# Optimization experiments

Measured on AMD Instinct MI355X. Metric: run time of the kernel, lower is better.

## Reference

```python
import jax, jax.numpy as jnp
import numpy as np

DROP_P = 0.1  # module default dropout


def setup_inputs() -> dict:
    key = jax.random.key(0)
    kq, kk, kv = jax.random.split(key, 3)
    B, L, H = 4, 4096, 64
    return {
        "q": jax.random.normal(kq, (B, L, H), dtype=jnp.float32),
        "k": jax.random.normal(kk, (B, L, H), dtype=jnp.float32),
        "v": jax.random.normal(kv, (B, L, H), dtype=jnp.float32),
    }


def reference(q, k, v):
    # q: [B, ql, H], k: [B, kl, H], v: [B, kl, H]
    H = q.shape[-1]
    scale = 1.0 / jnp.sqrt(jnp.asarray(H, dtype=q.dtype))
    # [B, ql, kl] score matrix (materialized, as in the original module)
    scores = jnp.einsum('bqh,bkh->bqk', q, k) * scale
    ql, kl = scores.shape[1], scores.shape[2]
    causal = jnp.tril(jnp.ones((ql, kl), dtype=bool))  # self.tril[:ql, :kl]
    scores = jnp.where(causal[None, :, :], scores, -jnp.inf)
    wei = jax.nn.softmax(scores, axis=-1)
    # deterministic dropout (train-mode path in the torch module)
    keep_p = 1.0 - DROP_P
    keep = jax.random.bernoulli(jax.random.key(42), keep_p, wei.shape)
    wei = jnp.where(keep, wei / keep_p, jnp.zeros((), dtype=wei.dtype))
    return jnp.einsum('bqk,bkh->bqh', wei, v)
```

## Files before the change

kernel.cpp:

```cpp
#include <hip/hip_runtime.h>

#define LQ   4096
#define HDIM 64
#define KEEP_LIMIT (7549747u << 9)
#define SCALE_LOG2E 0.18033688011112042f

typedef __attribute__((ext_vector_type(8))) short short8v;
typedef __attribute__((ext_vector_type(4))) short short4v;
typedef __attribute__((ext_vector_type(4))) float f32x4;

__device__ __forceinline__ unsigned rotl32(unsigned x, int r) {
  return (x << r) | (x >> (32 - r));
}

__device__ __forceinline__ float keep_sel(unsigned j, float e) {
  const unsigned ks1 = 42u;
  const unsigned ks2 = 0x1BD11BDAu ^ 42u;
  unsigned x0 = 0u, x1 = j + ks1;
#define TFR(r) { x0 += x1; x1 = rotl32(x1, r); x1 ^= x0; }
  TFR(13) TFR(15) TFR(26) TFR(6)   x0 += ks1; x1 += ks2 + 1u;
  TFR(17) TFR(29) TFR(16) TFR(24)  x0 += ks2; x1 += 0u  + 2u;
  TFR(13) TFR(15) TFR(26) TFR(6)   x0 += 0u;  x1 += ks1 + 3u;
  TFR(17) TFR(29) TFR(16) TFR(24)  x0 += ks1; x1 += ks2 + 4u;
  TFR(13) TFR(15) TFR(26) TFR(6)   x0 += ks2; x1 += 0u  + 5u;
#undef TFR
  return ((x0 ^ x1) < KEEP_LIMIT) ? e : 0.f;
}

__device__ __forceinline__ unsigned short f2bf(float x) {
  unsigned u = __float_as_uint(x);
  u += 0x7fffu + ((u >> 16) & 1u);
  return (unsigned short)(u >> 16);
}

__device__ __forceinline__ void gload16(const void* g, void* l) {
  __builtin_amdgcn_global_load_lds(
      (const __attribute__((address_space(1))) unsigned int*)g,
      (__attribute__((address_space(3))) unsigned int*)l, 16, 0, 0);
}

#if __has_builtin(__builtin_amdgcn_mfma_f32_16x16x16bf16_1k)
#define MFMA16(a, b, c) __builtin_amdgcn_mfma_f32_16x16x16bf16_1k(a, b, c, 0, 0, 0)
#else
__device__ __forceinline__ f32x4 mfma16_asm(short4v a, short4v b, f32x4 c) {
  f32x4 d;
  asm volatile("v_mfma_f32_16x16x16_bf16 %0, %1, %2, %3"
               : "=v"(d) : "v"(a), "v"(b), "v"(c));
  return d;
}
#define MFMA16(a, b, c) mfma16_asm(a, b, c)
#endif

__global__ __launch_bounds__(256) void prep(const float* __restrict__ k,
                                            const float* __restrict__ v,
                                            unsigned short* __restrict__ kb,
                                            unsigned short* __restrict__ vtb) {
  __shared__ float t[64][65];
  const int b = blockIdx.y, tl = blockIdx.x;
  const int tid = threadIdx.x, lane = tid & 63, grp = tid >> 6;
  {
    const float* kp = k + ((size_t)b * LQ + tl * 64) * HDIM;
    unsigned short* kbp = kb + ((size_t)b * LQ + tl * 64) * HDIM;
#pragma unroll
    for (int i = 0; i < 4; i++) {
      int e = (i * 256 + tid) * 4;
      float4 x = *(const float4*)(kp + e);
      ushort4 y;
      y.x = f2bf(x.x); y.y = f2bf(x.y); y.z = f2bf(x.z); y.w = f2bf(x.w);
      *(ushort4*)(kbp + e) = y;
    }
  }
#pragma unroll
  for (int c = 0; c < 16; c++) {
    int r = c * 4 + grp;
    t[r][lane] = v[((size_t)b * LQ + tl * 64 + r) * HDIM + lane];
  }
  __syncthreads();
#pragma unroll
  for (int c = 0; c < 16; c++) {
    int h = c * 4 + grp;
    vtb[((size_t)b * HDIM + h) * LQ + tl * 64 + lane] = f2bf(t[lane][h]);
  }
}

__global__ __launch_bounds__(256, 4) void attn(
    const float* __restrict__ q, const unsigned short* __restrict__ kb,
    const unsigned short* __restrict__ vtb, float* __restrict__ o,
    float* __restrict__ plsum) {
  __shared__ __align__(16) unsigned short vl[4][64 * 64];

  const int bx = blockIdx.x;
  const int tile16 = 255 - (bx >> 3);
  const int b = (bx >> 1) & 3;
  const int s = bx & 1;
  const int tid = threadIdx.x, lane = tid & 63, wq = tid >> 6;
  const int g = lane >> 4, r = lane & 15;
  const int qrow = tile16 * 16 + r;
  const int nt = (tile16 >> 2) + 1;
  const int half = (nt + 1) >> 1;
  const int ts = s ? half : 0, te = s ? nt : half;
  const int ntm1 = nt - 1;
  const unsigned sw = (unsigned)((r & 7) << 4);
  const unsigned jq = ((unsigned)b << 24) | ((unsigned)qrow << 12);
  const f32x4 zero4 = (f32x4){0.f, 0.f, 0.f, 0.f};

  short8v qf0, qf1;
  {
    const float* qp = q + ((size_t)b * LQ + qrow) * HDIM + g * 8;
    float4 a0 = *(const float4*)qp;
    float4 a1 = *(const float4*)(qp + 4);
    float4 b0 = *(const float4*)(qp + 32);
    float4 b1 = *(const float4*)(qp + 36);
    qf0[0] = (short)f2bf(a0.x); qf0[1] = (short)f2bf(a0.y);
    qf0[2] = (short)f2bf(a0.z); qf0[3] = (short)f2bf(a0.w);
    qf0[4] = (short)f2bf(a1.x); qf0[5] = (short)f2bf(a1.y);
    qf0[6] = (short)f2bf(a1.z); qf0[7] = (short)f2bf(a1.w);
    qf1[0] = (short)f2bf(b0.x); qf1[1] = (short)f2bf(b0.y);
    qf1[2] = (short)f2bf(b0.z); qf1[3] = (short)f2bf(b0.w);
    qf1[4] = (short)f2bf(b1.x); qf1[5] = (short)f2bf(b1.y);
    qf1[6] = (short)f2bf(b1.z); qf1[7] = (short)f2bf(b1.w);
  }

  const char* vt_b = (const char*)vtb + (size_t)b * HDIM * LQ * 2;
  const char* vpA;
  const char* vpB;
  {
    unsigned d0 = (unsigned)(tid * 16);
    unsigned d1 = d0 + 4096u;
    unsigned vsrc0 = (d0 >> 7) * (LQ * 2) + ((d0 & 127u) ^ (((d0 >> 7) & 7u) << 4));
    unsigned vsrc1 = (d1 >> 7) * (LQ * 2) + ((d1 & 127u) ^ (((d1 >> 7) & 7u) << 4));
    vpA = vt_b + vsrc0 + (size_t)ts * 128;
    vpB = vt_b + vsrc1 + (size_t)ts * 128;
  }
  const char* kp =
      (const char*)kb + ((size_t)b * LQ + wq * 16 + r) * 128 + g * 16 +
      (size_t)ts * 8192;

  char* const lw = (char*)&vl[0][0] + wq * 1024;

  f32x4 acc[4];
  acc[0] = zero4; acc[1] = zero4; acc[2] = zero4; acc[3] = zero4;
  float lsum = 0.f;

  const int n = te - ts;
  short8v kA0 = {}, kA1 = {}, kB0 = {}, kB1 = {};
  if (n > 0) {
    gload16(vpA, lw);
    gload16(vpB, lw + 4096);
    kA0 = *(const short8v*)(kp);
    kA1 = *(const short8v*)(kp + 64);
  }
  if (n > 1) {
    gload16(vpA + 128, lw + 8192);
    gload16(vpB + 128, lw + 8192 + 4096);
    kB0 = *(const short8v*)(kp + 8192);
    kB1 = *(const short8v*)(kp + 8192 + 64);
  }
  kp += 16384;
  __syncthreads();

#define COMPUTE_TILE(K0, K1, BUFI, T, DIAG)                                    \
  {                                                                            \
    const char* vlp = (const char*)&vl[BUFI][0] + r * 128 +                    \
                      (((unsigned)(wq * 32 + g * 8)) ^ sw);                    \
    short4v vf[4];                                                             \
    _Pragma("unroll") for (int hg = 0; hg < 4; ++hg)                           \
        vf[hg] = *(const short4v*)(vlp + hg * 2048);                           \
    f32x4 S = __builtin_amdgcn_mfma_f32_16x16x32_bf16(K0, qf0, zero4, 0, 0, 0);\
    S = __builtin_amdgcn_mfma_f32_16x16x32_bf16(K1, qf1, S, 0, 0, 0);          \
    const int kvb = (T) * 64 + wq * 16 + g * 4;                                \
    float w[4];                                                                \
    if (DIAG) {                                                                \
      _Pragma("unroll") for (int reg = 0; reg < 4; ++reg) {                    \
        float e = (kvb + reg <= qrow) ? exp2f(S[reg] * SCALE_LOG2E) : 0.f;     \
        lsum += e;                                                             \
        w[reg] = keep_sel(jq | (unsigned)(kvb + reg), e);                      \
      }                                                                        \
    } else {                                                                   \
      _Pragma("unroll") for (int reg = 0; reg < 4; ++reg) {                    \
        float e = exp2f(S[reg] * SCALE_LOG2E);                                 \
        lsum += e;                                                             \
        w[reg] = keep_sel(jq | (unsigned)(kvb + reg), e);                      \
      }                                                                        \
    }                                                                          \
    union { unsigned u[2]; short4v s4; } pu;                                   \
    asm("v_cvt_pk_bf16_f32 %0, %1, %2" : "=v"(pu.u[0]) : "v"(w[0]), "v"(w[1]));\
    asm("v_cvt_pk_bf16_f32 %0, %1, %2" : "=v"(pu.u[1]) : "v"(w[2]), "v"(w[3]));\
    const short4v pa = pu.s4;                                                  \
    _Pragma("unroll") for (int hg = 0; hg < 4; ++hg)                           \
        acc[hg] = MFMA16(pa, vf[hg], acc[hg]);                                 \
  }

  int t = ts;
  int base = 0;
  for (; t + 2 <= te; t += 2) {
    short8v nA0 = kA0, nA1 = kA1, nB0 = kB0, nB1 = kB1;
    char* const lwn = lw + (base ^ 2) * 8192;
    if (t + 2 < te) {
      gload16(vpA + 256, lwn);
      gload16(vpB + 256, lwn + 4096);
      nA0 = *(const short8v*)(kp);
      nA1 = *(const short8v*)(kp + 64);
    }
    if (t + 3 < te) {
      gload16(vpA + 384, lwn + 8192);
      gload16(vpB + 384, lwn + 8192 + 4096);
      nB0 = *(const short8v*)(kp + 8192);
      nB1 = *(const short8v*)(kp + 8192 + 64);
    }

    COMPUTE_TILE(kA0, kA1, base, t, false)
    COMPUTE_TILE(kB0, kB1, base + 1, t + 1, (t + 1) == ntm1)

    __syncthreads();
    kA0 = nA0; kA1 = nA1; kB0 = nB0; kB1 = nB1;
    vpA += 256; vpB += 256; kp += 16384;
    base ^= 2;
  }
  if (t < te) {
    COMPUTE_TILE(kA0, kA1, base, t, t == ntm1)
  }
#undef COMPUTE_TILE

  lsum += __shfl_xor(lsum, 16);
  lsum += __shfl_xor(lsum, 32);
  if (lane < 16)
    atomicAdd(&plsum[b * LQ + tile16 * 16 + lane], lsum);

  float* ob = o + ((size_t)b * LQ + tile16 * 16) * HDIM;
#pragma unroll
  for (int hg = 0; hg < 4; ++hg)
#pragma unroll
    for (int reg = 0; reg < 4; ++reg)
      atomicAdd(&ob[(g * 4 + reg) * HDIM + hg * 16 + r], acc[hg][reg]);
}

__global__ __launch_bounds__(256) void norm(float* __restrict__ o,
                                            const float* __restrict__ plsum) {
  const int idx = blockIdx.x * 256 + threadIdx.x;
  f32x4 x = ((const f32x4*)o)[idx];
  const float inv = 1.0f / (plsum[idx >> 4] * 0.9f);
  ((f32x4*)o)[idx] = x * inv;
}

extern "C" void kernel_launch(void* const* d_in, const int* in_sizes, int n_in,
                              void* d_out, int out_size, void* d_ws, size_t ws_size,
                              hipStream_t stream) {
  const float* q = (const float*)d_in[0];
  const float* k = (const float*)d_in[1];
  const float* v = (const float*)d_in[2];
  float* out = (float*)d_out;
  unsigned short* kb  = (unsigned short*)d_ws;
  unsigned short* vtb = kb + (size_t)4 * LQ * HDIM;
  float* plsum = (float*)((char*)d_ws + (size_t)4 * 1024 * 1024);

  hipMemsetAsync(out, 0, (size_t)4 * LQ * HDIM * sizeof(float), stream);
  hipMemsetAsync(plsum, 0, (size_t)4 * LQ * sizeof(float), stream);
  prep<<<dim3(64, 4), 256, 0, stream>>>(k, v, kb, vtb);
  attn<<<2048, 256, 0, stream>>>(q, kb, vtb, out, plsum);
  norm<<<1024, 256, 0, stream>>>(out, plsum);
}
```

Baseline: 96.67 us.

## Precompute dropout keep-mask as bitmask in a separate kernel

Moves the Threefry-based dropout keep decision out of the attention inner loop into a new mask_gen kernel. That kernel writes a packed triangular bitmask, one 64-bit ballot word per query row and 64-key block. The attention kernel now loads one mask word per tile and tests a nibble instead of running 20 hash rounds per element, which removes ALU work from the hot loop. In exchange it adds a kernel launch that still computes every hash, plus several MB of mask writes and reads. The mask is regenerated on every call, so no work is reused across calls.

```diff
diff --git a/kernel.cpp b/kernel.cpp
--- a/kernel.cpp
+++ b/kernel.cpp
@@ -4,6 +4,7 @@
 #define HDIM 64
 #define KEEP_LIMIT (7549747u << 9)
 #define SCALE_LOG2E 0.18033688011112042f
+#define MWORDS_PER_B 133120u
 
 typedef __attribute__((ext_vector_type(8))) short short8v;
 typedef __attribute__((ext_vector_type(4))) short short4v;
@@ -13,18 +14,9 @@
   return (x << r) | (x >> (32 - r));
 }
 
-__device__ __forceinline__ float keep_sel(unsigned j, float e) {
-  const unsigned ks1 = 42u;
-  const unsigned ks2 = 0x1BD11BDAu ^ 42u;
-  unsigned x0 = 0u, x1 = j + ks1;
-#define TFR(r) { x0 += x1; x1 = rotl32(x1, r); x1 ^= x0; }
-  TFR(13) TFR(15) TFR(26) TFR(6)   x0 += ks1; x1 += ks2 + 1u;
-  TFR(17) TFR(29) TFR(16) TFR(24)  x0 += ks2; x1 += 0u  + 2u;
-  TFR(13) TFR(15) TFR(26) TFR(6)   x0 += 0u;  x1 += ks1 + 3u;
-  TFR(17) TFR(29) TFR(16) TFR(24)  x0 += ks1; x1 += ks2 + 4u;
-  TFR(13) TFR(15) TFR(26) TFR(6)   x0 += ks2; x1 += 0u  + 5u;
-#undef TFR
-  return ((x0 ^ x1) < KEEP_LIMIT) ? e : 0.f;
+__device__ __forceinline__ unsigned tri_off(int q) {
+  unsigned g = (unsigned)q >> 6;
+  return 32u * g * (g + 1u) + ((unsigned)q - (g << 6)) * (g + 1u);
 }
 
 __device__ __forceinline__ unsigned short f2bf(float x) {
@@ -50,6 +42,33 @@
 }
 #define MFMA16(a, b, c) mfma16_asm(a, b, c)
 #endif
+
+__global__ __launch_bounds__(256) void mask_gen(
+    unsigned long long* __restrict__ mask) {
+  const int bx = blockIdx.x;
+  const int q = 4095 - (bx >> 2);
+  const int b = bx & 3;
+  const int lane = threadIdx.x & 63, wv = threadIdx.x >> 6;
+  const int nw = (q >> 6) + 1;
+  unsigned long long* mrow = mask + (size_t)b * MWORDS_PER_B + tri_off(q);
+  const unsigned jbase =
+      ((unsigned)b << 24) | ((unsigned)q << 12) | (unsigned)lane;
+  const unsigned ks1 = 42u;
+  const unsigned ks2 = 0x1BD11BDAu ^ 42u;
+
+  for (int wd = wv; wd < nw; wd += 4) {
+    unsigned x0 = 0u, x1 = jbase + (unsigned)(wd << 6) + ks1;
+#define TFR(r) { x0 += x1; x1 = rotl32(x1, r); x1 ^= x0; }
+    TFR(13) TFR(15) TFR(26) TFR(6)   x0 += ks1; x1 += ks2 + 1u;
+    TFR(17) TFR(29) TFR(16) TFR(24)  x0 += ks2; x1 += 0u  + 2u;
+    TFR(13) TFR(15) TFR(26) TFR(6)   x0 += 0u;  x1 += ks1 + 3u;
+    TFR(17) TFR(29) TFR(16) TFR(24)  x0 += ks1; x1 += ks2 + 4u;
+    TFR(13) TFR(15) TFR(26) TFR(6)   x0 += ks2; x1 += 0u  + 5u;
+#undef TFR
+    unsigned long long bal = __ballot((x0 ^ x1) < KEEP_LIMIT);
+    if (lane == 0) mrow[wd] = bal;
+  }
+}
 
 __global__ __launch_bounds__(256) void prep(const float* __restrict__ k,
                                             const float* __restrict__ v,
@@ -85,7 +104,8 @@
 
 __global__ __launch_bounds__(256, 4) void attn(
     const float* __restrict__ q, const unsigned short* __restrict__ kb,
-    const unsigned short* __restrict__ vtb, float* __restrict__ o,
+    const unsigned short* __restrict__ vtb,
+    const unsigned long long* __restrict__ mask, float* __restrict__ o,
     float* __restrict__ plsum) {
   __shared__ __align__(16) unsigned short vl[4][64 * 64];
 
@@ -101,8 +121,11 @@
   const int ts = s ? half : 0, te = s ? nt : half;
   const int ntm1 = nt - 1;
   const unsigned sw = (unsigned)((r & 7) << 4);
-  const unsigned jq = ((unsigned)b << 24) | ((unsigned)qrow << 12);
+  const unsigned msh = (unsigned)(wq * 16 + g * 4);
   const f32x4 zero4 = (f32x4){0.f, 0.f, 0.f, 0.f};
+
+  const unsigned long long* mwp =
+      mask + (size_t)b * MWORDS_PER_B + tri_off(qrow);
 
   short8v qf0, qf1;
   {
@@ -144,23 +167,28 @@
 
   const int n = te - ts;
   short8v kA0 = {}, kA1 = {}, kB0 = {}, kB1 = {};
+  unsigned long long mA = 0, mB = 0;
   if (n > 0) {
     gload16(vpA, lw);
     gload16(vpB, lw + 4096);
     kA0 = *(const short8v*)(kp);
     kA1 = *(const short8v*)(kp + 64);
+    mA = mwp[ts];
   }
   if (n > 1) {
     gload16(vpA + 128, lw + 8192);
     gload16(vpB + 128, lw + 8192 + 4096);
     kB0 = *(const short8v*)(kp + 8192);
     kB1 = *(const short8v*)(kp + 8192 + 64);
+    mB = mwp[ts + 1];
   }
   kp += 16384;
   __syncthreads();
 
-#define COMPUTE_TILE(K0, K1, BUFI, T, DIAG)                                    \
+#define COMPUTE_TILE(K0, K1, BUFI, T, DIAG, MW)                                \
   {                                                                            \
+    const int kvb = (T) * 64 + wq * 16 + g * 4;                                \
+    const unsigned nib = (unsigned)((MW) >> msh) & 15u;                        \
     const char* vlp = (const char*)&vl[BUFI][0] + r * 128 +                    \
                       (((unsigned)(wq * 32 + g * 8)) ^ sw);                    \
     short4v vf[4];                                                             \
@@ -168,19 +196,18 @@
         vf[hg] = *(const short4v*)(vlp + hg * 2048);                           \
     f32x4 S = __builtin_amdgcn_mfma_f32_16x16x32_bf16(K0, qf0, zero4, 0, 0, 0);\
     S = __builtin_amdgcn_mfma_f32_16x16x32_bf16(K1, qf1, S, 0, 0, 0);          \
-    const int kvb = (T) * 64 + wq * 16 + g * 4;                                \
     float w[4];                                                                \
     if (DIAG) {                                                                \
       _Pragma("unroll") for (int reg = 0; reg < 4; ++reg) {                    \
         float e = (kvb + reg <= qrow) ? exp2f(S[reg] * SCALE_LOG2E) : 0.f;     \
         lsum += e;                                                             \
-        w[reg] = keep_sel(jq | (unsigned)(kvb + reg), e);                      \
+        w[reg] = (nib & (1u << reg)) ? e : 0.f;                                \
       }                                                                        \
     } else {                                                                   \
       _Pragma("unroll") for (int reg = 0; reg < 4; ++reg) {                    \
         float e = exp2f(S[reg] * SCALE_LOG2E);                                 \
         lsum += e;                                                             \
-        w[reg] = keep_sel(jq | (unsigned)(kvb + reg), e);                      \
+        w[reg] = (nib & (1u << reg)) ? e : 0.f;                                \
       }                                                                        \
     }                                                                          \
     union { unsigned u[2]; short4v s4; } pu;                                   \
@@ -195,30 +222,34 @@
   int base = 0;
   for (; t + 2 <= te; t += 2) {
     short8v nA0 = kA0, nA1 = kA1, nB0 = kB0, nB1 = kB1;
+    unsigned long long nmA = mA, nmB = mB;
     char* const lwn = lw + (base ^ 2) * 8192;
     if (t + 2 < te) {
       gload16(vpA + 256, lwn);
       gload16(vpB + 256, lwn + 4096);
       nA0 = *(const short8v*)(kp);
       nA1 = *(const short8v*)(kp + 64);
+      nmA = mwp[t + 2];
     }
     if (t + 3 < te) {
       gload16(vpA + 384, lwn + 8192);
       gload16(vpB + 384, lwn + 8192 + 4096);
       nB0 = *(const short8v*)(kp + 8192);
       nB1 = *(const short8v*)(kp + 8192 + 64);
+      nmB = mwp[t + 3];
     }
 
-    COMPUTE_TILE(kA0, kA1, base, t, false)
-    COMPUTE_TILE(kB0, kB1, base + 1, t + 1, (t + 1) == ntm1)
+    COMPUTE_TILE(kA0, kA1, base, t, false, mA)
+    COMPUTE_TILE(kB0, kB1, base + 1, t + 1, (t + 1) == ntm1, mB)
 
     __syncthreads();
     kA0 = nA0; kA1 = nA1; kB0 = nB0; kB1 = nB1;
+    mA = nmA; mB = nmB;
     vpA += 256; vpB += 256; kp += 16384;
     base ^= 2;
   }
   if (t < te) {
-    COMPUTE_TILE(kA0, kA1, base, t, t == ntm1)
+    COMPUTE_TILE(kA0, kA1, base, t, t == ntm1, mA)
   }
 #undef COMPUTE_TILE
 
@@ -252,11 +283,15 @@
   float* out = (float*)d_out;
   unsigned short* kb  = (unsigned short*)d_ws;
   unsigned short* vtb = kb + (size_t)4 * LQ * HDIM;
-  float* plsum = (float*)((char*)d_ws + (size_t)4 * 1024 * 1024);
+  unsigned long long* mask =
+      (unsigned long long*)((char*)d_ws + (size_t)4 * 1024 * 1024);
+  float* plsum = (float*)((char*)d_ws + (size_t)4 * 1024 * 1024 +
+                          (size_t)4 * MWORDS_PER_B * 8);
 
   hipMemsetAsync(out, 0, (size_t)4 * LQ * HDIM * sizeof(float), stream);
   hipMemsetAsync(plsum, 0, (size_t)4 * LQ * sizeof(float), stream);
+  mask_gen<<<16384, 256, 0, stream>>>(mask);
   prep<<<dim3(64, 4), 256, 0, stream>>>(k, v, kb, vtb);
-  attn<<<2048, 256, 0, stream>>>(q, kb, vtb, out, plsum);
+  attn<<<2048, 256, 0, stream>>>(q, kb, vtb, mask, out, plsum);
   norm<<<1024, 256, 0, stream>>>(out, plsum);
 }
```

After: 160.8 us. 1.66x slower.

## Drop split-KV atomics and fuse normalization into attention epilogue

Applied to the files above, without the earlier changes.

Each block now processes the full causal key range for its 16-row query tile instead of splitting it across two blocks. The four waves' partial outputs and row sums are reduced in shared memory and normalized in place before a single vectorized store. This removes the two memsets, the global atomics and the separate normalization kernel. In exchange the grid is halved, and the longest blocks (diagonal tiles near the end) now carry twice the work, which can worsen load imbalance and tail latency.

```diff
diff --git a/kernel.cpp b/kernel.cpp
--- a/kernel.cpp
+++ b/kernel.cpp
@@ -85,20 +85,17 @@
 
 __global__ __launch_bounds__(256, 4) void attn(
     const float* __restrict__ q, const unsigned short* __restrict__ kb,
-    const unsigned short* __restrict__ vtb, float* __restrict__ o,
-    float* __restrict__ plsum) {
+    const unsigned short* __restrict__ vtb, float* __restrict__ o) {
   __shared__ __align__(16) unsigned short vl[4][64 * 64];
+  __shared__ float lsq[4][16];
 
   const int bx = blockIdx.x;
-  const int tile16 = 255 - (bx >> 3);
-  const int b = (bx >> 1) & 3;
-  const int s = bx & 1;
+  const int tile16 = 255 - (bx >> 2);
+  const int b = bx & 3;
   const int tid = threadIdx.x, lane = tid & 63, wq = tid >> 6;
   const int g = lane >> 4, r = lane & 15;
   const int qrow = tile16 * 16 + r;
   const int nt = (tile16 >> 2) + 1;
-  const int half = (nt + 1) >> 1;
-  const int ts = s ? half : 0, te = s ? nt : half;
   const int ntm1 = nt - 1;
   const unsigned sw = (unsigned)((r & 7) << 4);
   const unsigned jq = ((unsigned)b << 24) | ((unsigned)qrow << 12);
@@ -129,12 +126,11 @@
     unsigned d1 = d0 + 4096u;
     unsigned vsrc0 = (d0 >> 7) * (LQ * 2) + ((d0 & 127u) ^ (((d0 >> 7) & 7u) << 4));
     unsigned vsrc1 = (d1 >> 7) * (LQ * 2) + ((d1 & 127u) ^ (((d1 >> 7) & 7u) << 4));
-    vpA = vt_b + vsrc0 + (size_t)ts * 128;
-    vpB = vt_b + vsrc1 + (size_t)ts * 128;
+    vpA = vt_b + vsrc0;
+    vpB = vt_b + vsrc1;
   }
   const char* kp =
-      (const char*)kb + ((size_t)b * LQ + wq * 16 + r) * 128 + g * 16 +
-      (size_t)ts * 8192;
+      (const char*)kb + ((size_t)b * LQ + wq * 16 + r) * 128 + g * 16;
 
   char* const lw = (char*)&vl[0][0] + wq * 1024;
 
@@ -142,15 +138,14 @@
   acc[0] = zero4; acc[1] = zero4; acc[2] = zero4; acc[3] = zero4;
   float lsum = 0.f;
 
-  const int n = te - ts;
   short8v kA0 = {}, kA1 = {}, kB0 = {}, kB1 = {};
-  if (n > 0) {
+  {
     gload16(vpA, lw);
     gload16(vpB, lw + 4096);
     kA0 = *(const short8v*)(kp);
     kA1 = *(const short8v*)(kp + 64);
   }
-  if (n > 1) {
+  if (nt > 1) {
     gload16(vpA + 128, lw + 8192);
     gload16(vpB + 128, lw + 8192 + 4096);
     kB0 = *(const short8v*)(kp + 8192);
@@ -191,18 +186,18 @@
         acc[hg] = MFMA16(pa, vf[hg], acc[hg]);                                 \
   }
 
-  int t = ts;
+  int t = 0;
   int base = 0;
-  for (; t + 2 <= te; t += 2) {
+  for (; t + 2 <= nt; t += 2) {
     short8v nA0 = kA0, nA1 = kA1, nB0 = kB0, nB1 = kB1;
     char* const lwn = lw + (base ^ 2) * 8192;
-    if (t + 2 < te) {
+    if (t + 2 < nt) {
       gload16(vpA + 256, lwn);
       gload16(vpB + 256, lwn + 4096);
       nA0 = *(const short8v*)(kp);
       nA1 = *(const short8v*)(kp + 64);
     }
-    if (t + 3 < te) {
+    if (t + 3 < nt) {
       gload16(vpA + 384, lwn + 8192);
       gload16(vpB + 384, lwn + 8192 + 4096);
       nB0 = *(const short8v*)(kp + 8192);
@@ -217,30 +212,34 @@
     vpA += 256; vpB += 256; kp += 16384;
     base ^= 2;
   }
-  if (t < te) {
+  if (t < nt) {
     COMPUTE_TILE(kA0, kA1, base, t, t == ntm1)
   }
 #undef COMPUTE_TILE
 
   lsum += __shfl_xor(lsum, 16);
   lsum += __shfl_xor(lsum, 32);
-  if (lane < 16)
-    atomicAdd(&plsum[b * LQ + tile16 * 16 + lane], lsum);
-
-  float* ob = o + ((size_t)b * LQ + tile16 * 16) * HDIM;
+  __syncthreads();
+  if (lane < 16) lsq[wq][lane] = lsum;
+  float* obuf = (float*)&vl[0][0];
 #pragma unroll
   for (int hg = 0; hg < 4; ++hg)
 #pragma unroll
     for (int reg = 0; reg < 4; ++reg)
-      atomicAdd(&ob[(g * 4 + reg) * HDIM + hg * 16 + r], acc[hg][reg]);
-}
-
-__global__ __launch_bounds__(256) void norm(float* __restrict__ o,
-                                            const float* __restrict__ plsum) {
-  const int idx = blockIdx.x * 256 + threadIdx.x;
-  f32x4 x = ((const f32x4*)o)[idx];
-  const float inv = 1.0f / (plsum[idx >> 4] * 0.9f);
-  ((f32x4*)o)[idx] = x * inv;
+      obuf[(wq * 16 + g * 4 + reg) * 64 + hg * 16 + r] = acc[hg][reg];
+  __syncthreads();
+
+  const int i = tid >> 4, h4 = tid & 15;
+  f32x4 vs = (f32x4){0, 0, 0, 0};
+#pragma unroll
+  for (int qq = 0; qq < 4; ++qq)
+    vs += *(const f32x4*)&obuf[(qq * 16 + i) * 64 + h4 * 4];
+  float ls = lsq[0][i] + lsq[1][i] + lsq[2][i] + lsq[3][i];
+  float inv = 1.0f / (ls * 0.9f);
+  float4 outv;
+  outv.x = vs[0] * inv; outv.y = vs[1] * inv;
+  outv.z = vs[2] * inv; outv.w = vs[3] * inv;
+  *(float4*)&o[((size_t)b * LQ + tile16 * 16 + i) * HDIM + h4 * 4] = outv;
 }
 
 extern "C" void kernel_launch(void* const* d_in, const int* in_sizes, int n_in,
@@ -252,11 +251,7 @@
   float* out = (float*)d_out;
   unsigned short* kb  = (unsigned short*)d_ws;
   unsigned short* vtb = kb + (size_t)4 * LQ * HDIM;
-  float* plsum = (float*)((char*)d_ws + (size_t)4 * 1024 * 1024);
-
-  hipMemsetAsync(out, 0, (size_t)4 * LQ * HDIM * sizeof(float), stream);
-  hipMemsetAsync(plsum, 0, (size_t)4 * LQ * sizeof(float), stream);
+
   prep<<<dim3(64, 4), 256, 0, stream>>>(k, v, kb, vtb);
-  attn<<<2048, 256, 0, stream>>>(q, kb, vtb, out, plsum);
-  norm<<<1024, 256, 0, stream>>>(out, plsum);
-}
+  attn<<<1024, 256, 0, stream>>>(q, kb, vtb, out);
+}
```

Result: slower. 103.9 us (+7.5%).

## Load V fragments directly from global into registers, dropping LDS staging

Applied to the files above, without the earlier changes.

Drops the LDS double buffer for the transposed V tiles, which was filled with global_load_lds. Each lane now loads its short4 V fragments straight from global memory into registers, prefetched one tile-pair ahead like K. This removes the per-iteration __syncthreads and the LDS traffic. With LDS freed, the occupancy hint is raised from 4 to 5 blocks per SM. The cost is narrower 8-byte uncoalesced-ish global loads per lane and more live registers for the V prefetch.

```diff
diff --git a/kernel.cpp b/kernel.cpp
--- a/kernel.cpp
+++ b/kernel.cpp
@@ -33,12 +33,6 @@
   return (unsigned short)(u >> 16);
 }
 
-__device__ __forceinline__ void gload16(const void* g, void* l) {
-  __builtin_amdgcn_global_load_lds(
-      (const __attribute__((address_space(1))) unsigned int*)g,
-      (__attribute__((address_space(3))) unsigned int*)l, 16, 0, 0);
-}
-
 #if __has_builtin(__builtin_amdgcn_mfma_f32_16x16x16bf16_1k)
 #define MFMA16(a, b, c) __builtin_amdgcn_mfma_f32_16x16x16bf16_1k(a, b, c, 0, 0, 0)
 #else
@@ -83,12 +77,10 @@
   }
 }
 
-__global__ __launch_bounds__(256, 4) void attn(
+__global__ __launch_bounds__(256, 5) void attn(
     const float* __restrict__ q, const unsigned short* __restrict__ kb,
     const unsigned short* __restrict__ vtb, float* __restrict__ o,
     float* __restrict__ plsum) {
-  __shared__ __align__(16) unsigned short vl[4][64 * 64];
-
   const int bx = blockIdx.x;
   const int tile16 = 255 - (bx >> 3);
   const int b = (bx >> 1) & 3;
@@ -100,7 +92,6 @@
   const int half = (nt + 1) >> 1;
   const int ts = s ? half : 0, te = s ? nt : half;
   const int ntm1 = nt - 1;
-  const unsigned sw = (unsigned)((r & 7) << 4);
   const unsigned jq = ((unsigned)b << 24) | ((unsigned)qrow << 12);
   const f32x4 zero4 = (f32x4){0.f, 0.f, 0.f, 0.f};
 
@@ -121,51 +112,36 @@
     qf1[6] = (short)f2bf(b1.z); qf1[7] = (short)f2bf(b1.w);
   }
 
-  const char* vt_b = (const char*)vtb + (size_t)b * HDIM * LQ * 2;
-  const char* vpA;
-  const char* vpB;
-  {
-    unsigned d0 = (unsigned)(tid * 16);
-    unsigned d1 = d0 + 4096u;
-    unsigned vsrc0 = (d0 >> 7) * (LQ * 2) + ((d0 & 127u) ^ (((d0 >> 7) & 7u) << 4));
-    unsigned vsrc1 = (d1 >> 7) * (LQ * 2) + ((d1 & 127u) ^ (((d1 >> 7) & 7u) << 4));
-    vpA = vt_b + vsrc0 + (size_t)ts * 128;
-    vpB = vt_b + vsrc1 + (size_t)ts * 128;
-  }
   const char* kp =
       (const char*)kb + ((size_t)b * LQ + wq * 16 + r) * 128 + g * 16 +
       (size_t)ts * 8192;
-
-  char* const lw = (char*)&vl[0][0] + wq * 1024;
+  const char* vp =
+      (const char*)vtb + ((size_t)b * HDIM + r) * (LQ * 2) +
+      (size_t)(wq * 16 + g * 4) * 2 + (size_t)ts * 128;
 
   f32x4 acc[4];
   acc[0] = zero4; acc[1] = zero4; acc[2] = zero4; acc[3] = zero4;
   float lsum = 0.f;
 
+#define LOADK(dst0, dst1, OFF)                                                 \
+  dst0 = *(const short8v*)(kp + (OFF));                                        \
+  dst1 = *(const short8v*)(kp + (OFF) + 64);
+#define LOADV(d0, d1, d2, d3, OFF)                                             \
+  d0 = *(const short4v*)(vp + (OFF));                                          \
+  d1 = *(const short4v*)(vp + (OFF) + 131072);                                 \
+  d2 = *(const short4v*)(vp + (OFF) + 262144);                                 \
+  d3 = *(const short4v*)(vp + (OFF) + 393216);
+
   const int n = te - ts;
   short8v kA0 = {}, kA1 = {}, kB0 = {}, kB1 = {};
-  if (n > 0) {
-    gload16(vpA, lw);
-    gload16(vpB, lw + 4096);
-    kA0 = *(const short8v*)(kp);
-    kA1 = *(const short8v*)(kp + 64);
-  }
-  if (n > 1) {
-    gload16(vpA + 128, lw + 8192);
-    gload16(vpB + 128, lw + 8192 + 4096);
-    kB0 = *(const short8v*)(kp + 8192);
-    kB1 = *(const short8v*)(kp + 8192 + 64);
-  }
-  kp += 16384;
-  __syncthreads();
-
-#define COMPUTE_TILE(K0, K1, BUFI, T, DIAG)                                    \
+  short4v vA0 = {}, vA1 = {}, vA2 = {}, vA3 = {};
+  short4v vB0 = {}, vB1 = {}, vB2 = {}, vB3 = {};
+  if (n > 0) { LOADK(kA0, kA1, 0) LOADV(vA0, vA1, vA2, vA3, 0) }
+  if (n > 1) { LOADK(kB0, kB1, 8192) LOADV(vB0, vB1, vB2, vB3, 128) }
+  kp += 16384; vp += 256;
+
+#define COMPUTE_TILE(K0, K1, V0, V1, V2, V3, T, DIAG)                          \
   {                                                                            \
-    const char* vlp = (const char*)&vl[BUFI][0] + r * 128 +                    \
-                      (((unsigned)(wq * 32 + g * 8)) ^ sw);                    \
-    short4v vf[4];                                                             \
-    _Pragma("unroll") for (int hg = 0; hg < 4; ++hg)                           \
-        vf[hg] = *(const short4v*)(vlp + hg * 2048);                           \
     f32x4 S = __builtin_amdgcn_mfma_f32_16x16x32_bf16(K0, qf0, zero4, 0, 0, 0);\
     S = __builtin_amdgcn_mfma_f32_16x16x32_bf16(K1, qf1, S, 0, 0, 0);          \
     const int kvb = (T) * 64 + wq * 16 + g * 4;                                \
@@ -187,40 +163,34 @@
     asm("v_cvt_pk_bf16_f32 %0, %1, %2" : "=v"(pu.u[0]) : "v"(w[0]), "v"(w[1]));\
     asm("v_cvt_pk_bf16_f32 %0, %1, %2" : "=v"(pu.u[1]) : "v"(w[2]), "v"(w[3]));\
     const short4v pa = pu.s4;                                                  \
-    _Pragma("unroll") for (int hg = 0; hg < 4; ++hg)                           \
-        acc[hg] = MFMA16(pa, vf[hg], acc[hg]);                                 \
+    acc[0] = MFMA16(pa, V0, acc[0]);                                           \
+    acc[1] = MFMA16(pa, V1, acc[1]);                                           \
+    acc[2] = MFMA16(pa, V2, acc[2]);                                           \
+    acc[3] = MFMA16(pa, V3, acc[3]);                                           \
   }
 
   int t = ts;
-  int base = 0;
   for (; t + 2 <= te; t += 2) {
     short8v nA0 = kA0, nA1 = kA1, nB0 = kB0, nB1 = kB1;
-    char* const lwn = lw + (base ^ 2) * 8192;
-    if (t + 2 < te) {
-      gload16(vpA + 256, lwn);
-      gload16(vpB + 256, lwn + 4096);
-      nA0 = *(const short8v*)(kp);
-      nA1 = *(const short8v*)(kp + 64);
-    }
-    if (t + 3 < te) {
-      gload16(vpA + 384, lwn + 8192);
-      gload16(vpB + 384, lwn + 8192 + 4096);
-      nB0 = *(const short8v*)(kp + 8192);
-      nB1 = *(const short8v*)(kp + 8192 + 64);
-    }
-
-    COMPUTE_TILE(kA0, kA1, base, t, false)
-    COMPUTE_TILE(kB0, kB1, base + 1, t + 1, (t + 1) == ntm1)
-
-    __syncthreads();
+    short4v nvA0 = vA0, nvA1 = vA1, nvA2 = vA2, nvA3 = vA3;
+    short4v nvB0 = vB0, nvB1 = vB1, nvB2 = vB2, nvB3 = vB3;
+    if (t + 2 < te) { LOADK(nA0, nA1, 0) LOADV(nvA0, nvA1, nvA2, nvA3, 0) }
+    if (t + 3 < te) { LOADK(nB0, nB1, 8192) LOADV(nvB0, nvB1, nvB2, nvB3, 128) }
+
+    COMPUTE_TILE(kA0, kA1, vA0, vA1, vA2, vA3, t, false)
+    COMPUTE_TILE(kB0, kB1, vB0, vB1, vB2, vB3, t + 1, (t + 1) == ntm1)
+
     kA0 = nA0; kA1 = nA1; kB0 = nB0; kB1 = nB1;
-    vpA += 256; vpB += 256; kp += 16384;
-    base ^= 2;
+    vA0 = nvA0; vA1 = nvA1; vA2 = nvA2; vA3 = nvA3;
+    vB0 = nvB0; vB1 = nvB1; vB2 = nvB2; vB3 = nvB3;
+    kp += 16384; vp += 256;
   }
   if (t < te) {
-    COMPUTE_TILE(kA0, kA1, base, t, t == ntm1)
+    COMPUTE_TILE(kA0, kA1, vA0, vA1, vA2, vA3, t, t == ntm1)
   }
 #undef COMPUTE_TILE
+#undef LOADK
+#undef LOADV
 
   lsum += __shfl_xor(lsum, 16);
   lsum += __shfl_xor(lsum, 32);
```

Measured after the change: 126.0 us. +30.3%, slower.
